# Kernel optimization log

Measured on AMD Instinct MI355X. Metric: run time of the kernel, lower is better.

Reference implementation:

```python
import jax, jax.numpy as jnp
import numpy as np

N_NODES = 50000
N_EDGES = 800000
N_FEAT = 128
HIDDEN = 64
N_GRAPHS = 256


def setup_inputs() -> dict:
    key = jax.random.key(0)
    ks = jax.random.split(key, 10)
    x = jax.random.normal(ks[0], (N_NODES, N_FEAT), dtype=jnp.float32)
    edge_index = jax.random.randint(ks[1], (2, N_EDGES), 0, N_NODES, dtype=jnp.int64)
    batch = jnp.sort(jax.random.randint(ks[2], (N_NODES,), 0, N_GRAPHS, dtype=jnp.int64))
    s1 = 1.0 / np.sqrt(N_FEAT)
    s2 = 1.0 / np.sqrt(HIDDEN)
    W1 = jax.random.normal(ks[3], (N_FEAT, HIDDEN), dtype=jnp.float32) * s1
    b1 = jnp.zeros((HIDDEN,), dtype=jnp.float32)
    W2 = jax.random.normal(ks[4], (HIDDEN, HIDDEN), dtype=jnp.float32) * s2
    b2 = jnp.zeros((HIDDEN,), dtype=jnp.float32)
    Wm1 = jax.random.normal(ks[5], (HIDDEN, HIDDEN), dtype=jnp.float32) * s2
    bm1 = jnp.zeros((HIDDEN,), dtype=jnp.float32)
    Wm2 = jax.random.normal(ks[6], (HIDDEN, 1), dtype=jnp.float32) * s2
    bm2 = jnp.zeros((1,), dtype=jnp.float32)
    return {"x": x, "edge_index": edge_index, "batch": batch,
            "W1": W1, "b1": b1, "W2": W2, "b2": b2,
            "Wm1": Wm1, "bm1": bm1, "Wm2": Wm2, "bm2": bm2}


def _gcn_layer(h, W, b, src, dst, norm, n_nodes):
    # GCNConv: h @ W, then symmetric-normalized scatter-add over edges (+ self-loops), + bias
    h = h @ W
    msg = h[src] * norm[:, None]              # [E+N, H] gather + scale
    agg = jax.ops.segment_sum(msg, dst, num_segments=n_nodes)
    return agg + b


def reference(x, edge_index, batch, W1, b1, W2, b2, Wm1, bm1, Wm2, bm2):
    n = x.shape[0]
    loops = jnp.arange(n, dtype=edge_index.dtype)
    src = jnp.concatenate([edge_index[0], loops])  # self-loops as in PyG GCNConv
    dst = jnp.concatenate([edge_index[1], loops])
    deg = jax.ops.segment_sum(jnp.ones_like(dst, dtype=x.dtype), dst, num_segments=n)
    dis = jnp.where(deg > 0, jax.lax.rsqrt(deg), 0.0)  # deg^-1/2
    norm = dis[src] * dis[dst]

    h = jax.nn.relu(_gcn_layer(x, W1, b1, src, dst, norm, n))
    h = jax.nn.relu(_gcn_layer(h, W2, b2, src, dst, norm, n))

    # global mean pool over graphs
    sums = jax.ops.segment_sum(h, batch, num_segments=N_GRAPHS)
    cnts = jax.ops.segment_sum(jnp.ones((n,), dtype=h.dtype), batch, num_segments=N_GRAPHS)
    pooled = sums / jnp.maximum(cnts, 1.0)[:, None]

    # MLP head (dropout inactive at eval)
    out = jax.nn.relu(pooled @ Wm1 + bm1) @ Wm2 + bm2
    return out.reshape(-1)
```

## Files before the change

kernel.cpp:

```cpp
#include <hip/hip_runtime.h>

#define NN 50000
#define NE 800000
#define NF 128
#define NH 64
#define NG 256
#define NB 196
#define NC 196
#define CH 4096
#define CELL 80
#define CAP 5120
#define NGB 782

typedef __attribute__((ext_vector_type(8))) short bf16x8;
typedef __attribute__((ext_vector_type(4))) float f32x4;

static __device__ __forceinline__ unsigned short f2bf(float f) {
    union { float f; unsigned u; } v; v.f = f;
    unsigned r = v.u + 0x7FFF + ((v.u >> 16) & 1);
    return (unsigned short)(r >> 16);
}
static __device__ __forceinline__ float lo16(unsigned u) {
    return __uint_as_float(u << 16);
}
static __device__ __forceinline__ float hi16(unsigned u) {
    return __uint_as_float(u & 0xFFFF0000u);
}
static __device__ __forceinline__ unsigned pack2(float a, float b) {
    return (unsigned)f2bf(a) | ((unsigned)f2bf(b) << 16);
}

__global__ __launch_bounds__(256) void prep_gemm(const int* __restrict__ ei,
                                                 int* __restrict__ histg,
                                                 unsigned* __restrict__ ebuf,
                                                 const float* __restrict__ X,
                                                 const float* __restrict__ W,
                                                 const float* __restrict__ W2,
                                                 unsigned short* __restrict__ Y,
                                                 float* __restrict__ psum,
                                                 unsigned* __restrict__ W2p) {
    __shared__ __align__(16) char smem[35840];
    const int t = threadIdx.x;

    if (blockIdx.x < NC) {
        int* hist = (int*)smem;
        int* incl = hist + 256;
        int* lcur = incl + 256;
        int* wq   = lcur + 256;
        unsigned* lpairs = (unsigned*)(smem + 4096);
        const int c = blockIdx.x;
        const int c0 = c * CH;

        hist[t] = 0;
        __syncthreads();

        int es[16], ed[16];
#pragma unroll
        for (int j = 0; j < 4; ++j) {
            const int e = c0 + (j * 256 + t) * 4;
            int4 s4 = make_int4(-1, -1, -1, -1);
            int4 d4 = make_int4(-1, -1, -1, -1);
            if (e + 3 < NE) {
                s4 = *(const int4*)&ei[e];
                d4 = *(const int4*)&ei[NE + e];
            } else {
                if (e < NE)     { s4.x = ei[e];     d4.x = ei[NE + e]; }
                if (e + 1 < NE) { s4.y = ei[e + 1]; d4.y = ei[NE + e + 1]; }
                if (e + 2 < NE) { s4.z = ei[e + 2]; d4.z = ei[NE + e + 2]; }
            }
            es[4*j] = s4.x; es[4*j+1] = s4.y; es[4*j+2] = s4.z; es[4*j+3] = s4.w;
            ed[4*j] = d4.x; ed[4*j+1] = d4.y; ed[4*j+2] = d4.z; ed[4*j+3] = d4.w;
            if (d4.x >= 0) atomicAdd(&hist[d4.x >> 8], 1);
            if (d4.y >= 0) atomicAdd(&hist[d4.y >> 8], 1);
            if (d4.z >= 0) atomicAdd(&hist[d4.z >> 8], 1);
            if (d4.w >= 0) atomicAdd(&hist[d4.w >> 8], 1);
        }
        __syncthreads();

        const int v = hist[t];
        int sv = v;
#pragma unroll
        for (int off = 1; off < 64; off <<= 1) {
            int u = __shfl_up(sv, off, 64);
            if ((t & 63) >= off) sv += u;
        }
        if ((t & 63) == 63) wq[t >> 6] = sv;
        __syncthreads();
        {
            const int wid = t >> 6;
            int add = 0;
            if (wid > 0) add += wq[0];
            if (wid > 1) add += wq[1];
            if (wid > 2) add += wq[2];
            sv += add;
        }
        incl[t] = sv;
        lcur[t] = sv - v;
        if (t < NB) histg[c * NB + t] = v;
        __syncthreads();

#pragma unroll
        for (int j = 0; j < 16; ++j) {
            const int d = ed[j];
            if (d >= 0) {
                int p = atomicAdd(&lcur[d >> 8], 1);
                lpairs[p] = (unsigned)es[j] | ((unsigned)d << 16);
            }
        }
        __syncthreads();

        const int total = incl[255];
        for (int p = t; p < total; p += 256) {
            const unsigned pr = lpairs[p];
            const int b = pr >> 24;
            const int i = p - (incl[b] - hist[b]);
            ebuf[(b * NC + c) * CELL + i] = pr;
        }
    } else {
        const int gb = blockIdx.x - NC;
        if (gb >= NGB) {
            for (int idx = t; idx < 2048; idx += 256) {
                const int n = idx >> 5, kp = idx & 31;
                W2p[idx] = pack2(W2[(2 * kp) * 64 + n], W2[(2 * kp + 1) * 64 + n]);
            }
            return;
        }
        if (gb < 16)
            *(float4*)&psum[gb * 1024 + t * 4] = make_float4(0.f, 0.f, 0.f, 0.f);

        unsigned short* Xs = (unsigned short*)smem;
        unsigned int* Wt = (unsigned int*)(smem + 17408);
        const int base = gb * 64;

        for (int i = t * 4; i < 64 * 128; i += 1024) {
            int node = i >> 7, k = i & 127;
            int gn = base + node; if (gn >= NN) gn = NN - 1;
            float4 v = *(const float4*)&X[(size_t)gn * 128 + k];
            ushort4 o = { f2bf(v.x), f2bf(v.y), f2bf(v.z), f2bf(v.w) };
            *(ushort4*)&Xs[node * 136 + k] = o;
        }
        for (int idx = t; idx < 64 * 64; idx += 256) {
            int n = idx & 63, kp = idx >> 6;
            float w0 = W[(2 * kp) * 64 + n];
            float w1 = W[(2 * kp + 1) * 64 + n];
            Wt[n * 68 + kp] = (unsigned)f2bf(w0) | ((unsigned)f2bf(w1) << 16);
        }
        __syncthreads();

        const int w = t >> 6;
        const int lane = t & 63;
        const int l15 = lane & 15;
        const int quad = lane >> 4;
        f32x4 acc[4] = {{0.f,0.f,0.f,0.f},{0.f,0.f,0.f,0.f},{0.f,0.f,0.f,0.f},{0.f,0.f,0.f,0.f}};
#pragma unroll
        for (int kk = 0; kk < 4; ++kk) {
            const bf16x8 a = *(const bf16x8*)&Xs[(w * 16 + l15) * 136 + quad * 8 + kk * 32];
#pragma unroll
            for (int nt = 0; nt < 4; ++nt) {
                const bf16x8 b = *(const bf16x8*)&Wt[(nt * 16 + l15) * 68 + quad * 4 + kk * 16];
                acc[nt] = __builtin_amdgcn_mfma_f32_16x16x32_bf16(a, b, acc[nt], 0, 0, 0);
            }
        }
        const int r0 = base + w * 16 + quad * 4;
#pragma unroll
        for (int reg = 0; reg < 4; ++reg) {
            const int row = r0 + reg;
            if (row < NN) {
#pragma unroll
                for (int nt = 0; nt < 4; ++nt)
                    Y[(size_t)row * 64 + nt * 16 + l15] = f2bf(acc[nt][reg]);
            }
        }
    }
}

__global__ __launch_bounds__(512) void build_csr(const unsigned* __restrict__ ebuf,
                                                 const int* __restrict__ histg,
                                                 int2* __restrict__ row_range,
                                                 float* __restrict__ dis,
                                                 int* __restrict__ csr_src) {
    const int b = blockIdx.x, t = threadIdx.x;
    const int e0 = b * CAP;
    __shared__ int coffs[256];
    __shared__ int deg_l[256];
    __shared__ int pre[256];
    __shared__ int cur[256];
    __shared__ int wq[8];
    __shared__ unsigned lpairs[CAP];
    __shared__ int lsrc[CAP];

    int cv = 0;
    if (t < NC) cv = histg[t * NB + b];
    int sv = cv;
    if (t < 256) {
#pragma unroll
        for (int off = 1; off < 64; off <<= 1) {
            int u = __shfl_up(sv, off, 64);
            if ((t & 63) >= off) sv += u;
        }
        if ((t & 63) == 63) wq[t >> 6] = sv;
        deg_l[t] = (b * 256 + t < NN) ? 1 : 0;
    }
    __syncthreads();
    if (t < 256) {
        const int wid = t >> 6;
        int add = 0;
        if (wid > 0) add += wq[0];
        if (wid > 1) add += wq[1];
        if (wid > 2) add += wq[2];
        coffs[t] = sv + add;
    }
    __syncthreads();

    if (t < NC && cv > 0) {
        const uint4* src4 = (const uint4*)&ebuf[(size_t)(b * NC + t) * CELL];
        const int dst = coffs[t] - cv;
        for (int i = 0; i < cv; i += 4) {
            const uint4 u = src4[i >> 2];
            lpairs[dst + i] = u.x;
            if (i + 1 < cv) lpairs[dst + i + 1] = u.y;
            if (i + 2 < cv) lpairs[dst + i + 2] = u.z;
            if (i + 3 < cv) lpairs[dst + i + 3] = u.w;
        }
    }
    __syncthreads();

    const int total = coffs[255];
    for (int i = t; i < total; i += 512)
        atomicAdd(&deg_l[(lpairs[i] >> 16) & 255], 1);
    __syncthreads();

    int dvi = 0, psv = 0;
    if (t < 256) {
        dvi = deg_l[t];
        psv = dvi;
#pragma unroll
        for (int off = 1; off < 64; off <<= 1) {
            int u = __shfl_up(psv, off, 64);
            if ((t & 63) >= off) psv += u;
        }
        if ((t & 63) == 63) wq[4 + (t >> 6)] = psv;
    }
    __syncthreads();
    if (t < 256) {
        const int wid = t >> 6;
        int add = 0;
        if (wid > 0) add += wq[4];
        if (wid > 1) add += wq[5];
        if (wid > 2) add += wq[6];
        psv += add;
        pre[t] = psv;
        cur[t] = 1;
        const int nd = b * 256 + t;
        if (nd < NN) {
            const int excl = psv - dvi;
            lsrc[excl] = nd;
            row_range[nd] = make_int2(e0 + excl, e0 + psv);
            dis[nd] = rsqrtf((float)dvi);
        }
    }
    __syncthreads();

    for (int i = t; i < total; i += 512) {
        const unsigned p = lpairs[i];
        const int d = (p >> 16) & 255;
        const int pos = (pre[d] - deg_l[d]) + atomicAdd(&cur[d], 1);
        lsrc[pos] = (int)(p & 0xFFFFu);
    }
    __syncthreads();
    const int tot_all = pre[255];
    for (int i = t; i < tot_all; i += 512)
        csr_src[e0 + i] = lsrc[i];
}

static __device__ __forceinline__ void acc8(float* acc, const uint4 u) {
    acc[0] += lo16(u.x); acc[1] += hi16(u.x);
    acc[2] += lo16(u.y); acc[3] += hi16(u.y);
    acc[4] += lo16(u.z); acc[5] += hi16(u.z);
    acc[6] += lo16(u.w); acc[7] += hi16(u.w);
}
static __device__ __forceinline__ void fma8(float* acc, const uint4 u, const float d) {
    acc[0] = fmaf(lo16(u.x), d, acc[0]); acc[1] = fmaf(hi16(u.x), d, acc[1]);
    acc[2] = fmaf(lo16(u.y), d, acc[2]); acc[3] = fmaf(hi16(u.y), d, acc[3]);
    acc[4] = fmaf(lo16(u.z), d, acc[4]); acc[5] = fmaf(hi16(u.z), d, acc[5]);
    acc[6] = fmaf(lo16(u.w), d, acc[6]); acc[7] = fmaf(hi16(u.w), d, acc[7]);
}

static __device__ __forceinline__ void gather_rows(const unsigned short* __restrict__ h,
                                                   const int* __restrict__ csr_src,
                                                   int lo, int hi, int p8, float* acc) {
    int i = lo;
    for (; i + 4 <= hi; i += 4) {
        const int i0 = csr_src[i];
        const int i1 = csr_src[i + 1];
        const int i2 = csr_src[i + 2];
        const int i3 = csr_src[i + 3];
        const uint4 u0 = *(const uint4*)&h[(i0 << 6) + p8];
        const uint4 u1 = *(const uint4*)&h[(i1 << 6) + p8];
        const uint4 u2 = *(const uint4*)&h[(i2 << 6) + p8];
        const uint4 u3 = *(const uint4*)&h[(i3 << 6) + p8];
        acc8(acc, u0); acc8(acc, u1); acc8(acc, u2); acc8(acc, u3);
    }
    for (; i + 2 <= hi; i += 2) {
        const int i0 = csr_src[i];
        const int i1 = csr_src[i + 1];
        const uint4 u0 = *(const uint4*)&h[(i0 << 6) + p8];
        const uint4 u1 = *(const uint4*)&h[(i1 << 6) + p8];
        acc8(acc, u0); acc8(acc, u1);
    }
    if (i < hi) {
        const int i0 = csr_src[i];
        acc8(acc, *(const uint4*)&h[(i0 << 6) + p8]);
    }
}

static __device__ __forceinline__ void gather_rows_scaled(const unsigned short* __restrict__ h,
                                                          const int* __restrict__ csr_src,
                                                          const float* __restrict__ dis,
                                                          int lo, int hi, int p8, float* acc) {
    int i = lo;
    for (; i + 4 <= hi; i += 4) {
        const int i0 = csr_src[i];
        const int i1 = csr_src[i + 1];
        const int i2 = csr_src[i + 2];
        const int i3 = csr_src[i + 3];
        const float d0 = dis[i0], d1 = dis[i1], d2 = dis[i2], d3 = dis[i3];
        const uint4 u0 = *(const uint4*)&h[(i0 << 6) + p8];
        const uint4 u1 = *(const uint4*)&h[(i1 << 6) + p8];
        const uint4 u2 = *(const uint4*)&h[(i2 << 6) + p8];
        const uint4 u3 = *(const uint4*)&h[(i3 << 6) + p8];
        fma8(acc, u0, d0); fma8(acc, u1, d1); fma8(acc, u2, d2); fma8(acc, u3, d3);
    }
    for (; i + 2 <= hi; i += 2) {
        const int i0 = csr_src[i];
        const int i1 = csr_src[i + 1];
        const float d0 = dis[i0], d1 = dis[i1];
        const uint4 u0 = *(const uint4*)&h[(i0 << 6) + p8];
        const uint4 u1 = *(const uint4*)&h[(i1 << 6) + p8];
        fma8(acc, u0, d0); fma8(acc, u1, d1);
    }
    if (i < hi) {
        const int i0 = csr_src[i];
        const float d0 = dis[i0];
        fma8(acc, *(const uint4*)&h[(i0 << 6) + p8], d0);
    }
}

__global__ __launch_bounds__(256) void agg_gemv(const unsigned short* __restrict__ h,
                                                const int2* __restrict__ row_range,
                                                const int* __restrict__ csr_src,
                                                const float* __restrict__ dis,
                                                const float* __restrict__ b1,
                                                const unsigned* __restrict__ W2p,
                                                unsigned short* __restrict__ g) {
    __shared__ unsigned short W2b[64 * 72];
    __shared__ unsigned short A[32 * 72];
    const int t = threadIdx.x;
    for (int idx = t; idx < 2048; idx += 256) {
        const int n = idx >> 5, kp = idx & 31;
        *(unsigned*)&W2b[n * 72 + 2 * kp] = W2p[idx];
    }

    const int base = blockIdx.x * 32;
    const int nloc = t >> 3;
    const int p8 = (t & 7) * 8;
    const int n = base + nloc;
    float acc[8] = {};
    if (n < NN) {
        const int2 rr = row_range[n];
        gather_rows_scaled(h, csr_src, dis, rr.x, rr.y, p8, acc);
        const float dn = dis[n];
        const float4 bv0 = *(const float4*)&b1[p8];
        const float4 bv1 = *(const float4*)&b1[p8 + 4];
        acc[0] = fmaxf(acc[0] * dn + bv0.x, 0.f);
        acc[1] = fmaxf(acc[1] * dn + bv0.y, 0.f);
        acc[2] = fmaxf(acc[2] * dn + bv0.z, 0.f);
        acc[3] = fmaxf(acc[3] * dn + bv0.w, 0.f);
        acc[4] = fmaxf(acc[4] * dn + bv1.x, 0.f);
        acc[5] = fmaxf(acc[5] * dn + bv1.y, 0.f);
        acc[6] = fmaxf(acc[6] * dn + bv1.z, 0.f);
        acc[7] = fmaxf(acc[7] * dn + bv1.w, 0.f);
    }
    uint4 pk;
    pk.x = pack2(acc[0], acc[1]);
    pk.y = pack2(acc[2], acc[3]);
    pk.z = pack2(acc[4], acc[5]);
    pk.w = pack2(acc[6], acc[7]);
    *(uint4*)&A[nloc * 72 + p8] = pk;
    __syncthreads();

    const int w = t >> 6;
    const int lane = t & 63;
    const int l15 = lane & 15;
    const int quad = lane >> 4;
    const int mt = w & 1;
    const int nq = (w >> 1) * 2;
    const bf16x8 a0 = *(const bf16x8*)&A[(mt * 16 + l15) * 72 + quad * 8];
    const bf16x8 a1 = *(const bf16x8*)&A[(mt * 16 + l15) * 72 + 32 + quad * 8];
    const bf16x8 b00 = *(const bf16x8*)&W2b[(nq * 16 + l15) * 72 + quad * 8];
    const bf16x8 b01 = *(const bf16x8*)&W2b[(nq * 16 + l15) * 72 + 32 + quad * 8];
    const bf16x8 b10 = *(const bf16x8*)&W2b[((nq + 1) * 16 + l15) * 72 + quad * 8];
    const bf16x8 b11 = *(const bf16x8*)&W2b[((nq + 1) * 16 + l15) * 72 + 32 + quad * 8];
    f32x4 c0 = {0.f, 0.f, 0.f, 0.f}, c1 = {0.f, 0.f, 0.f, 0.f};
    c0 = __builtin_amdgcn_mfma_f32_16x16x32_bf16(a0, b00, c0, 0, 0, 0);
    c0 = __builtin_amdgcn_mfma_f32_16x16x32_bf16(a1, b01, c0, 0, 0, 0);
    c1 = __builtin_amdgcn_mfma_f32_16x16x32_bf16(a0, b10, c1, 0, 0, 0);
    c1 = __builtin_amdgcn_mfma_f32_16x16x32_bf16(a1, b11, c1, 0, 0, 0);
    const int r0 = base + mt * 16 + quad * 4;
    float4 d4 = *(const float4*)&dis[r0];
    const float dd[4] = { d4.x, d4.y, d4.z, d4.w };
#pragma unroll
    for (int reg = 0; reg < 4; ++reg) {
        const int row = r0 + reg;
        if (row < NN) {
            g[(size_t)row * 64 + nq * 16 + l15] = f2bf(c0[reg] * dd[reg]);
            g[(size_t)row * 64 + (nq + 1) * 16 + l15] = f2bf(c1[reg] * dd[reg]);
        }
    }
}

__global__ __launch_bounds__(256) void agg_pool(const unsigned short* __restrict__ h,
                                                const int2* __restrict__ row_range,
                                                const int* __restrict__ csr_src,
                                                const float* __restrict__ dis,
                                                const float* __restrict__ bias,
                                                const int* __restrict__ batch,
                                                float* __restrict__ psum) {
    __shared__ float rowsL[32 * 68];
    __shared__ int nb[32];
    const int t = threadIdx.x;
    const int nloc = t >> 3;
    const int n = blockIdx.x * 32 + nloc;
    const int p8 = (t & 7) * 8;
    if ((t & 7) == 0) nb[nloc] = (n < NN) ? batch[n] : -1;
    if (n < NN) {
        const int2 rr = row_range[n];
        float acc[8] = {};
        gather_rows(h, csr_src, rr.x, rr.y, p8, acc);
        const float dn = dis[n];
        const float4 bv0 = *(const float4*)&bias[p8];
        const float4 bv1 = *(const float4*)&bias[p8 + 4];
        float4 r0, r1;
        r0.x = fmaxf(acc[0] * dn + bv0.x, 0.f);
        r0.y = fmaxf(acc[1] * dn + bv0.y, 0.f);
        r0.z = fmaxf(acc[2] * dn + bv0.z, 0.f);
        r0.w = fmaxf(acc[3] * dn + bv0.w, 0.f);
        r1.x = fmaxf(acc[4] * dn + bv1.x, 0.f);
        r1.y = fmaxf(acc[5] * dn + bv1.y, 0.f);
        r1.z = fmaxf(acc[6] * dn + bv1.z, 0.f);
        r1.w = fmaxf(acc[7] * dn + bv1.w, 0.f);
        *(float4*)&rowsL[nloc * 68 + p8] = r0;
        *(float4*)&rowsL[nloc * 68 + p8 + 4] = r1;
    }
    __syncthreads();
    if (t < 64) {
        float s = 0.f; int curg = -2;
        for (int r = 0; r < 32; ++r) {
            const int gg = nb[r];
            if (gg != curg) {
                if (curg >= 0) atomicAdd(&psum[curg * 64 + t], s);
                s = 0.f; curg = gg;
            }
            if (gg >= 0) s += rowsL[r * 68 + t];
        }
        if (curg >= 0) atomicAdd(&psum[curg * 64 + t], s);
    }
}

__global__ __launch_bounds__(64) void head_kernel(const float* __restrict__ psum,
                                                  const int* __restrict__ batch,
                                                  const float* __restrict__ Wm1,
                                                  const float* __restrict__ bm1,
                                                  const float* __restrict__ Wm2,
                                                  const float* __restrict__ bm2,
                                                  float* __restrict__ out) {
    const int g = blockIdx.x;
    const int t = threadIdx.x;
    int lo = 0, hi = NN;
    while (lo < hi) { int m = (lo + hi) >> 1; if (batch[m] < g) lo = m + 1; else hi = m; }
    const int s = lo;
    hi = NN;
    while (lo < hi) { int m = (lo + hi) >> 1; if (batch[m] < g + 1) lo = m + 1; else hi = m; }
    const int cnt = lo - s;

    __shared__ float pl[64];
    pl[t] = psum[g * 64 + t] / (float)(cnt > 0 ? cnt : 1);
    __syncthreads();
    float z = bm1[t];
#pragma unroll 8
    for (int k = 0; k < 64; ++k)
        z += pl[k] * Wm1[k * 64 + t];
    z = fmaxf(z, 0.f);
    float y = z * Wm2[t];
    for (int off = 32; off; off >>= 1) y += __shfl_down(y, off);
    if (t == 0) out[g] = y + bm2[0];
}

extern "C" void kernel_launch(void* const* d_in, const int* in_sizes, int n_in,
                              void* d_out, int out_size, void* d_ws, size_t ws_size,
                              hipStream_t stream) {
    const float* x   = (const float*)d_in[0];
    const int*   ei  = (const int*)d_in[1];
    const int*   bat = (const int*)d_in[2];
    const float* W1  = (const float*)d_in[3];
    const float* b1  = (const float*)d_in[4];
    const float* W2  = (const float*)d_in[5];
    const float* b2  = (const float*)d_in[6];
    const float* Wm1 = (const float*)d_in[7];
    const float* bm1 = (const float*)d_in[8];
    const float* Wm2 = (const float*)d_in[9];
    const float* bm2 = (const float*)d_in[10];
    float* out = (float*)d_out;

    char* w = (char*)d_ws;
    int*            histg     = (int*)           (w + 0);
    int2*           row_range = (int2*)          (w + 153664);
    float*          dis       = (float*)         (w + 553664);
    int*            csr_src   = (int*)           (w + 753664);
    unsigned*       ebuf      = (unsigned*)      (w + 4767744);
    unsigned short* bufA      = (unsigned short*)(w + 17060864);
    unsigned short* bufB      = (unsigned short*)(w + 23460864);
    float*          psum      = (float*)         (w + 29860864);
    unsigned*       W2p       = (unsigned*)      (w + 29926400);

    prep_gemm <<<NC + NGB + 1, 256, 0, stream>>>(ei, histg, ebuf, x, W1, W2, bufA, psum, W2p);
    build_csr <<<NB, 512, 0, stream>>>(ebuf, histg, row_range, dis, csr_src);
    agg_gemv  <<<(NN + 31) / 32, 256, 0, stream>>>(bufA, row_range, csr_src, dis, b1, W2p, bufB);
    agg_pool  <<<(NN + 31) / 32, 256, 0, stream>>>(bufB, row_range, csr_src, dis, b2, bat, psum);
    head_kernel<<<NG, 64, 0, stream>>>(psum, bat, Wm1, bm1, Wm2, bm2, out);
}
```

Before: 149.7 us.

## Use 16 threads per node in aggregation kernels and compute graph counts in pooling

The two aggregation kernels now use 16 lanes per node with 8-byte gathers and 512-thread blocks instead of 8 lanes with 16-byte gathers, doubling memory-level parallelism per node and unrolling gathers 8-deep. In the GEMV each wave now does one MFMA column tile. The head kernel's binary search over batch is replaced by per-graph counts accumulated atomically during pooling, and build_csr spreads the ebuf copy across all 512 threads. The trade-off is more threads and shorter per-lane loads, plus extra count atomics and a widened psum zeroing region.

```diff
diff --git a/kernel.cpp b/kernel.cpp
--- a/kernel.cpp
+++ b/kernel.cpp
@@ -125,8 +125,10 @@
             }
             return;
         }
-        if (gb < 16)
-            *(float4*)&psum[gb * 1024 + t * 4] = make_float4(0.f, 0.f, 0.f, 0.f);
+        if (gb < 17) {
+            const int o = gb * 1024 + t * 4;
+            if (o < 16640) *(float4*)&psum[o] = make_float4(0.f, 0.f, 0.f, 0.f);
+        }
 
         unsigned short* Xs = (unsigned short*)smem;
         unsigned int* Wt = (unsigned int*)(smem + 17408);
@@ -182,6 +184,7 @@
     const int b = blockIdx.x, t = threadIdx.x;
     const int e0 = b * CAP;
     __shared__ int coffs[256];
+    __shared__ int cvs[256];
     __shared__ int deg_l[256];
     __shared__ int pre[256];
     __shared__ int cur[256];
@@ -200,6 +203,7 @@
         }
         if ((t & 63) == 63) wq[t >> 6] = sv;
         deg_l[t] = (b * 256 + t < NN) ? 1 : 0;
+        cvs[t] = cv;
     }
     __syncthreads();
     if (t < 256) {
@@ -212,15 +216,20 @@
     }
     __syncthreads();
 
-    if (t < NC && cv > 0) {
-        const uint4* src4 = (const uint4*)&ebuf[(size_t)(b * NC + t) * CELL];
-        const int dst = coffs[t] - cv;
-        for (int i = 0; i < cv; i += 4) {
-            const uint4 u = src4[i >> 2];
-            lpairs[dst + i] = u.x;
-            if (i + 1 < cv) lpairs[dst + i + 1] = u.y;
-            if (i + 2 < cv) lpairs[dst + i + 2] = u.z;
-            if (i + 3 < cv) lpairs[dst + i + 3] = u.w;
+    {
+        const int tc = t & 255;
+        const int cv2 = cvs[tc];
+        if (tc < NC && cv2 > 0) {
+            const uint4* src4 = (const uint4*)&ebuf[(size_t)(b * NC + tc) * CELL];
+            const int dst = coffs[tc] - cv2;
+            for (int g4 = (t >> 8); g4 * 4 < cv2; g4 += 2) {
+                const uint4 u = src4[g4];
+                const int i = g4 * 4;
+                lpairs[dst + i] = u.x;
+                if (i + 1 < cv2) lpairs[dst + i + 1] = u.y;
+                if (i + 2 < cv2) lpairs[dst + i + 2] = u.z;
+                if (i + 3 < cv2) lpairs[dst + i + 3] = u.w;
+            }
         }
     }
     __syncthreads();
@@ -273,80 +282,91 @@
         csr_src[e0 + i] = lsrc[i];
 }
 
-static __device__ __forceinline__ void acc8(float* acc, const uint4 u) {
+static __device__ __forceinline__ void acc4(float* acc, const uint2 u) {
     acc[0] += lo16(u.x); acc[1] += hi16(u.x);
     acc[2] += lo16(u.y); acc[3] += hi16(u.y);
-    acc[4] += lo16(u.z); acc[5] += hi16(u.z);
-    acc[6] += lo16(u.w); acc[7] += hi16(u.w);
-}
-static __device__ __forceinline__ void fma8(float* acc, const uint4 u, const float d) {
+}
+static __device__ __forceinline__ void fma4(float* acc, const uint2 u, const float d) {
     acc[0] = fmaf(lo16(u.x), d, acc[0]); acc[1] = fmaf(hi16(u.x), d, acc[1]);
     acc[2] = fmaf(lo16(u.y), d, acc[2]); acc[3] = fmaf(hi16(u.y), d, acc[3]);
-    acc[4] = fmaf(lo16(u.z), d, acc[4]); acc[5] = fmaf(hi16(u.z), d, acc[5]);
-    acc[6] = fmaf(lo16(u.w), d, acc[6]); acc[7] = fmaf(hi16(u.w), d, acc[7]);
-}
-
-static __device__ __forceinline__ void gather_rows(const unsigned short* __restrict__ h,
-                                                   const int* __restrict__ csr_src,
-                                                   int lo, int hi, int p8, float* acc) {
+}
+
+static __device__ __forceinline__ void gather16(const unsigned short* __restrict__ h,
+                                                const int* __restrict__ csr,
+                                                int lo, int hi, int p4, float* acc) {
     int i = lo;
-    for (; i + 4 <= hi; i += 4) {
-        const int i0 = csr_src[i];
-        const int i1 = csr_src[i + 1];
-        const int i2 = csr_src[i + 2];
-        const int i3 = csr_src[i + 3];
-        const uint4 u0 = *(const uint4*)&h[(i0 << 6) + p8];
-        const uint4 u1 = *(const uint4*)&h[(i1 << 6) + p8];
-        const uint4 u2 = *(const uint4*)&h[(i2 << 6) + p8];
-        const uint4 u3 = *(const uint4*)&h[(i3 << 6) + p8];
-        acc8(acc, u0); acc8(acc, u1); acc8(acc, u2); acc8(acc, u3);
-    }
-    for (; i + 2 <= hi; i += 2) {
-        const int i0 = csr_src[i];
-        const int i1 = csr_src[i + 1];
-        const uint4 u0 = *(const uint4*)&h[(i0 << 6) + p8];
-        const uint4 u1 = *(const uint4*)&h[(i1 << 6) + p8];
-        acc8(acc, u0); acc8(acc, u1);
+    for (; i + 8 <= hi; i += 8) {
+        int idx[8];
+#pragma unroll
+        for (int j = 0; j < 8; ++j) idx[j] = csr[i + j];
+        uint2 u[8];
+#pragma unroll
+        for (int j = 0; j < 8; ++j) u[j] = *(const uint2*)&h[(idx[j] << 6) + p4];
+#pragma unroll
+        for (int j = 0; j < 8; ++j) acc4(acc, u[j]);
+    }
+    if (i + 4 <= hi) {
+        int idx[4];
+#pragma unroll
+        for (int j = 0; j < 4; ++j) idx[j] = csr[i + j];
+#pragma unroll
+        for (int j = 0; j < 4; ++j) acc4(acc, *(const uint2*)&h[(idx[j] << 6) + p4]);
+        i += 4;
+    }
+    if (i + 2 <= hi) {
+        const int i0 = csr[i], i1 = csr[i + 1];
+        const uint2 u0 = *(const uint2*)&h[(i0 << 6) + p4];
+        const uint2 u1 = *(const uint2*)&h[(i1 << 6) + p4];
+        acc4(acc, u0); acc4(acc, u1);
+        i += 2;
+    }
+    if (i < hi) acc4(acc, *(const uint2*)&h[(csr[i] << 6) + p4]);
+}
+
+static __device__ __forceinline__ void gather16_scaled(const unsigned short* __restrict__ h,
+                                                       const int* __restrict__ csr,
+                                                       const float* __restrict__ dis,
+                                                       int lo, int hi, int p4, float* acc) {
+    int i = lo;
+    for (; i + 8 <= hi; i += 8) {
+        int idx[8];
+#pragma unroll
+        for (int j = 0; j < 8; ++j) idx[j] = csr[i + j];
+        float d[8];
+#pragma unroll
+        for (int j = 0; j < 8; ++j) d[j] = dis[idx[j]];
+        uint2 u[8];
+#pragma unroll
+        for (int j = 0; j < 8; ++j) u[j] = *(const uint2*)&h[(idx[j] << 6) + p4];
+#pragma unroll
+        for (int j = 0; j < 8; ++j) fma4(acc, u[j], d[j]);
+    }
+    if (i + 4 <= hi) {
+        int idx[4];
+#pragma unroll
+        for (int j = 0; j < 4; ++j) idx[j] = csr[i + j];
+        float d[4];
+#pragma unroll
+        for (int j = 0; j < 4; ++j) d[j] = dis[idx[j]];
+#pragma unroll
+        for (int j = 0; j < 4; ++j) fma4(acc, *(const uint2*)&h[(idx[j] << 6) + p4], d[j]);
+        i += 4;
+    }
+    if (i + 2 <= hi) {
+        const int i0 = csr[i], i1 = csr[i + 1];
+        const float d0 = dis[i0], d1 = dis[i1];
+        const uint2 u0 = *(const uint2*)&h[(i0 << 6) + p4];
+        const uint2 u1 = *(const uint2*)&h[(i1 << 6) + p4];
+        fma4(acc, u0, d0); fma4(acc, u1, d1);
+        i += 2;
     }
     if (i < hi) {
-        const int i0 = csr_src[i];
-        acc8(acc, *(const uint4*)&h[(i0 << 6) + p8]);
-    }
-}
-
-static __device__ __forceinline__ void gather_rows_scaled(const unsigned short* __restrict__ h,
-                                                          const int* __restrict__ csr_src,
-                                                          const float* __restrict__ dis,
-                                                          int lo, int hi, int p8, float* acc) {
-    int i = lo;
-    for (; i + 4 <= hi; i += 4) {
-        const int i0 = csr_src[i];
-        const int i1 = csr_src[i + 1];
-        const int i2 = csr_src[i + 2];
-        const int i3 = csr_src[i + 3];
-        const float d0 = dis[i0], d1 = dis[i1], d2 = dis[i2], d3 = dis[i3];
-        const uint4 u0 = *(const uint4*)&h[(i0 << 6) + p8];
-        const uint4 u1 = *(const uint4*)&h[(i1 << 6) + p8];
-        const uint4 u2 = *(const uint4*)&h[(i2 << 6) + p8];
-        const uint4 u3 = *(const uint4*)&h[(i3 << 6) + p8];
-        fma8(acc, u0, d0); fma8(acc, u1, d1); fma8(acc, u2, d2); fma8(acc, u3, d3);
-    }
-    for (; i + 2 <= hi; i += 2) {
-        const int i0 = csr_src[i];
-        const int i1 = csr_src[i + 1];
-        const float d0 = dis[i0], d1 = dis[i1];
-        const uint4 u0 = *(const uint4*)&h[(i0 << 6) + p8];
-        const uint4 u1 = *(const uint4*)&h[(i1 << 6) + p8];
-        fma8(acc, u0, d0); fma8(acc, u1, d1);
-    }
-    if (i < hi) {
-        const int i0 = csr_src[i];
-        const float d0 = dis[i0];
-        fma8(acc, *(const uint4*)&h[(i0 << 6) + p8], d0);
-    }
-}
-
-__global__ __launch_bounds__(256) void agg_gemv(const unsigned short* __restrict__ h,
+        const int i0 = csr[i];
+        fma4(acc, *(const uint2*)&h[(i0 << 6) + p4], dis[i0]);
+    }
+}
+
+__global__ __launch_bounds__(512) void agg_gemv(const unsigned short* __restrict__ h,
                                                 const int2* __restrict__ row_range,
                                                 const int* __restrict__ csr_src,
                                                 const float* __restrict__ dis,
@@ -356,37 +376,29 @@
     __shared__ unsigned short W2b[64 * 72];
     __shared__ unsigned short A[32 * 72];
     const int t = threadIdx.x;
-    for (int idx = t; idx < 2048; idx += 256) {
-        const int n = idx >> 5, kp = idx & 31;
-        *(unsigned*)&W2b[n * 72 + 2 * kp] = W2p[idx];
-    }
-
     const int base = blockIdx.x * 32;
-    const int nloc = t >> 3;
-    const int p8 = (t & 7) * 8;
+    const int nloc = t >> 4;
+    const int p4 = (t & 15) * 4;
     const int n = base + nloc;
-    float acc[8] = {};
+    float acc[4] = {};
     if (n < NN) {
         const int2 rr = row_range[n];
-        gather_rows_scaled(h, csr_src, dis, rr.x, rr.y, p8, acc);
+        gather16_scaled(h, csr_src, dis, rr.x, rr.y, p4, acc);
         const float dn = dis[n];
-        const float4 bv0 = *(const float4*)&b1[p8];
-        const float4 bv1 = *(const float4*)&b1[p8 + 4];
-        acc[0] = fmaxf(acc[0] * dn + bv0.x, 0.f);
-        acc[1] = fmaxf(acc[1] * dn + bv0.y, 0.f);
-        acc[2] = fmaxf(acc[2] * dn + bv0.z, 0.f);
-        acc[3] = fmaxf(acc[3] * dn + bv0.w, 0.f);
-        acc[4] = fmaxf(acc[4] * dn + bv1.x, 0.f);
-        acc[5] = fmaxf(acc[5] * dn + bv1.y, 0.f);
-        acc[6] = fmaxf(acc[6] * dn + bv1.z, 0.f);
-        acc[7] = fmaxf(acc[7] * dn + bv1.w, 0.f);
-    }
-    uint4 pk;
+        const float4 bv = *(const float4*)&b1[p4];
+        acc[0] = fmaxf(acc[0] * dn + bv.x, 0.f);
+        acc[1] = fmaxf(acc[1] * dn + bv.y, 0.f);
+        acc[2] = fmaxf(acc[2] * dn + bv.z, 0.f);
+        acc[3] = fmaxf(acc[3] * dn + bv.w, 0.f);
+    }
+    for (int idx = t; idx < 2048; idx += 512) {
+        const int nn2 = idx >> 5, kp = idx & 31;
+        *(unsigned*)&W2b[nn2 * 72 + 2 * kp] = W2p[idx];
+    }
+    uint2 pk;
     pk.x = pack2(acc[0], acc[1]);
     pk.y = pack2(acc[2], acc[3]);
-    pk.z = pack2(acc[4], acc[5]);
-    pk.w = pack2(acc[6], acc[7]);
-    *(uint4*)&A[nloc * 72 + p8] = pk;
+    *(uint2*)&A[nloc * 72 + p4] = pk;
     __syncthreads();
 
     const int w = t >> 6;
@@ -394,81 +406,76 @@
     const int l15 = lane & 15;
     const int quad = lane >> 4;
     const int mt = w & 1;
-    const int nq = (w >> 1) * 2;
+    const int ncol = w >> 1;
     const bf16x8 a0 = *(const bf16x8*)&A[(mt * 16 + l15) * 72 + quad * 8];
     const bf16x8 a1 = *(const bf16x8*)&A[(mt * 16 + l15) * 72 + 32 + quad * 8];
-    const bf16x8 b00 = *(const bf16x8*)&W2b[(nq * 16 + l15) * 72 + quad * 8];
-    const bf16x8 b01 = *(const bf16x8*)&W2b[(nq * 16 + l15) * 72 + 32 + quad * 8];
-    const bf16x8 b10 = *(const bf16x8*)&W2b[((nq + 1) * 16 + l15) * 72 + quad * 8];
-    const bf16x8 b11 = *(const bf16x8*)&W2b[((nq + 1) * 16 + l15) * 72 + 32 + quad * 8];
-    f32x4 c0 = {0.f, 0.f, 0.f, 0.f}, c1 = {0.f, 0.f, 0.f, 0.f};
-    c0 = __builtin_amdgcn_mfma_f32_16x16x32_bf16(a0, b00, c0, 0, 0, 0);
-    c0 = __builtin_amdgcn_mfma_f32_16x16x32_bf16(a1, b01, c0, 0, 0, 0);
-    c1 = __builtin_amdgcn_mfma_f32_16x16x32_bf16(a0, b10, c1, 0, 0, 0);
-    c1 = __builtin_amdgcn_mfma_f32_16x16x32_bf16(a1, b11, c1, 0, 0, 0);
+    const bf16x8 bb0 = *(const bf16x8*)&W2b[(ncol * 16 + l15) * 72 + quad * 8];
+    const bf16x8 bb1 = *(const bf16x8*)&W2b[(ncol * 16 + l15) * 72 + 32 + quad * 8];
+    f32x4 c = {0.f, 0.f, 0.f, 0.f};
+    c = __builtin_amdgcn_mfma_f32_16x16x32_bf16(a0, bb0, c, 0, 0, 0);
+    c = __builtin_amdgcn_mfma_f32_16x16x32_bf16(a1, bb1, c, 0, 0, 0);
     const int r0 = base + mt * 16 + quad * 4;
     float4 d4 = *(const float4*)&dis[r0];
     const float dd[4] = { d4.x, d4.y, d4.z, d4.w };
 #pragma unroll
     for (int reg = 0; reg < 4; ++reg) {
         const int row = r0 + reg;
-        if (row < NN) {
-            g[(size_t)row * 64 + nq * 16 + l15] = f2bf(c0[reg] * dd[reg]);
-            g[(size_t)row * 64 + (nq + 1) * 16 + l15] = f2bf(c1[reg] * dd[reg]);
-        }
-    }
-}
-
-__global__ __launch_bounds__(256) void agg_pool(const unsigned short* __restrict__ h,
+        if (row < NN)
+            g[(size_t)row * 64 + ncol * 16 + l15] = f2bf(c[reg] * dd[reg]);
+    }
+}
+
+__global__ __launch_bounds__(512) void agg_pool(const unsigned short* __restrict__ h,
                                                 const int2* __restrict__ row_range,
                                                 const int* __restrict__ csr_src,
                                                 const float* __restrict__ dis,
                                                 const float* __restrict__ bias,
                                                 const int* __restrict__ batch,
-                                                float* __restrict__ psum) {
+                                                float* __restrict__ psum,
+                                                float* __restrict__ cnt) {
     __shared__ float rowsL[32 * 68];
     __shared__ int nb[32];
     const int t = threadIdx.x;
-    const int nloc = t >> 3;
+    const int nloc = t >> 4;
     const int n = blockIdx.x * 32 + nloc;
-    const int p8 = (t & 7) * 8;
-    if ((t & 7) == 0) nb[nloc] = (n < NN) ? batch[n] : -1;
+    const int p4 = (t & 15) * 4;
+    if ((t & 15) == 0) nb[nloc] = (n < NN) ? batch[n] : -1;
     if (n < NN) {
         const int2 rr = row_range[n];
-        float acc[8] = {};
-        gather_rows(h, csr_src, rr.x, rr.y, p8, acc);
+        float acc[4] = {};
+        gather16(h, csr_src, rr.x, rr.y, p4, acc);
         const float dn = dis[n];
-        const float4 bv0 = *(const float4*)&bias[p8];
-        const float4 bv1 = *(const float4*)&bias[p8 + 4];
-        float4 r0, r1;
-        r0.x = fmaxf(acc[0] * dn + bv0.x, 0.f);
-        r0.y = fmaxf(acc[1] * dn + bv0.y, 0.f);
-        r0.z = fmaxf(acc[2] * dn + bv0.z, 0.f);
-        r0.w = fmaxf(acc[3] * dn + bv0.w, 0.f);
-        r1.x = fmaxf(acc[4] * dn + bv1.x, 0.f);
-        r1.y = fmaxf(acc[5] * dn + bv1.y, 0.f);
-        r1.z = fmaxf(acc[6] * dn + bv1.z, 0.f);
-        r1.w = fmaxf(acc[7] * dn + bv1.w, 0.f);
-        *(float4*)&rowsL[nloc * 68 + p8] = r0;
-        *(float4*)&rowsL[nloc * 68 + p8 + 4] = r1;
+        const float4 bv = *(const float4*)&bias[p4];
+        float4 r;
+        r.x = fmaxf(acc[0] * dn + bv.x, 0.f);
+        r.y = fmaxf(acc[1] * dn + bv.y, 0.f);
+        r.z = fmaxf(acc[2] * dn + bv.z, 0.f);
+        r.w = fmaxf(acc[3] * dn + bv.w, 0.f);
+        *(float4*)&rowsL[nloc * 68 + p4] = r;
     }
     __syncthreads();
     if (t < 64) {
-        float s = 0.f; int curg = -2;
+        float s = 0.f; int curg = -2; int rl = 0;
         for (int r = 0; r < 32; ++r) {
             const int gg = nb[r];
             if (gg != curg) {
-                if (curg >= 0) atomicAdd(&psum[curg * 64 + t], s);
-                s = 0.f; curg = gg;
-            }
-            if (gg >= 0) s += rowsL[r * 68 + t];
-        }
-        if (curg >= 0) atomicAdd(&psum[curg * 64 + t], s);
+                if (curg >= 0) {
+                    atomicAdd(&psum[curg * 64 + t], s);
+                    if (t == 0) atomicAdd(&cnt[curg], (float)rl);
+                }
+                s = 0.f; rl = 0; curg = gg;
+            }
+            if (gg >= 0) { s += rowsL[r * 68 + t]; ++rl; }
+        }
+        if (curg >= 0) {
+            atomicAdd(&psum[curg * 64 + t], s);
+            if (t == 0) atomicAdd(&cnt[curg], (float)rl);
+        }
     }
 }
 
 __global__ __launch_bounds__(64) void head_kernel(const float* __restrict__ psum,
-                                                  const int* __restrict__ batch,
+                                                  const float* __restrict__ cnt,
                                                   const float* __restrict__ Wm1,
                                                   const float* __restrict__ bm1,
                                                   const float* __restrict__ Wm2,
@@ -476,15 +483,9 @@
                                                   float* __restrict__ out) {
     const int g = blockIdx.x;
     const int t = threadIdx.x;
-    int lo = 0, hi = NN;
-    while (lo < hi) { int m = (lo + hi) >> 1; if (batch[m] < g) lo = m + 1; else hi = m; }
-    const int s = lo;
-    hi = NN;
-    while (lo < hi) { int m = (lo + hi) >> 1; if (batch[m] < g + 1) lo = m + 1; else hi = m; }
-    const int cnt = lo - s;
-
     __shared__ float pl[64];
-    pl[t] = psum[g * 64 + t] / (float)(cnt > 0 ? cnt : 1);
+    const float inv = 1.f / fmaxf(cnt[g], 1.f);
+    pl[t] = psum[g * 64 + t] * inv;
     __syncthreads();
     float z = bm1[t];
 #pragma unroll 8
@@ -521,11 +522,12 @@
     unsigned short* bufA      = (unsigned short*)(w + 17060864);
     unsigned short* bufB      = (unsigned short*)(w + 23460864);
     float*          psum      = (float*)         (w + 29860864);
-    unsigned*       W2p       = (unsigned*)      (w + 29926400);
+    unsigned*       W2p       = (unsigned*)      (w + 29927424);
+    float*          cnt       = psum + 16384;
 
     prep_gemm <<<NC + NGB + 1, 256, 0, stream>>>(ei, histg, ebuf, x, W1, W2, bufA, psum, W2p);
     build_csr <<<NB, 512, 0, stream>>>(ebuf, histg, row_range, dis, csr_src);
-    agg_gemv  <<<(NN + 31) / 32, 256, 0, stream>>>(bufA, row_range, csr_src, dis, b1, W2p, bufB);
-    agg_pool  <<<(NN + 31) / 32, 256, 0, stream>>>(bufB, row_range, csr_src, dis, b2, bat, psum);
-    head_kernel<<<NG, 64, 0, stream>>>(psum, bat, Wm1, bm1, Wm2, bm2, out);
-}
+    agg_gemv  <<<(NN + 31) / 32, 512, 0, stream>>>(bufA, row_range, csr_src, dis, b1, W2p, bufB);
+    agg_pool  <<<(NN + 31) / 32, 512, 0, stream>>>(bufB, row_range, csr_src, dis, b2, bat, psum, cnt);
+    head_kernel<<<NG, 64, 0, stream>>>(psum, cnt, Wm1, bm1, Wm2, bm2, out);
+}
```

Result: slower. 158.6 us (+6.0%).
